# Optimization experiments

Measured on AMD Instinct MI355X. Metric: run time of the kernel, lower is better.

Reference implementation:

```python
import jax, jax.numpy as jnp
import numpy as np

WS = 32          # window_size; N = WS*WS tokens
NH = 8           # num_heads
HD = 64          # head_dim
DIM = 512        # model dim (= NH*HD)
B = 16
N = WS * WS


def _rel_index() -> np.ndarray:
    """Relative position index, identical to the torch __init__ construction."""
    coords = np.stack(np.meshgrid(np.arange(WS), np.arange(WS), indexing='ij'))
    coords = coords.reshape(2, -1)                       # [2, N]
    rel = coords[:, :, None] - coords[:, None, :]        # [2, N, N]
    rel = rel.transpose(1, 2, 0).copy()                  # [N, N, 2]
    rel[..., 0] += WS - 1
    rel[..., 1] += WS - 1
    rel[..., 0] *= 2 * WS - 1
    return rel.sum(-1).astype(np.int32)                  # [N, N], values in [0, (2WS-1)^2)


def setup_inputs() -> dict:
    key = jax.random.key(0)
    ks = jax.random.split(key, 5)
    s = DIM ** -0.5
    return {
        "x": jax.random.normal(ks[0], (B, N, DIM), jnp.float32),
        "qkv_w": jax.random.normal(ks[1], (3 * NH * HD, DIM), jnp.float32) * s,
        "qkv_b": jnp.zeros((3 * NH * HD,), jnp.float32),
        "proj_w": jax.random.normal(ks[2], (DIM, NH * HD), jnp.float32) * s,
        "proj_b": jnp.zeros((DIM,), jnp.float32),
        "bias_table": jax.random.normal(ks[3], ((2 * WS - 1) ** 2, NH), jnp.float32) * 0.02,
        "rel_index": jnp.asarray(_rel_index()),
    }


def reference(x, qkv_w, qkv_b, proj_w, proj_b, bias_table, rel_index):
    Bb, Nn, C = x.shape
    qkv = (x @ qkv_w.T + qkv_b).reshape(Bb, Nn, 3, NH, HD)
    q, k, v = jnp.moveaxis(qkv, 2, 0)                    # each [B, N, NH, HD]
    q = q * (HD ** -0.5)
    attn = jnp.einsum('bnhd,bmhd->bhnm', q, k)           # [B, NH, N, N]
    bias = bias_table[rel_index]                         # gather -> [N, N, NH]
    attn = attn + jnp.transpose(bias, (2, 0, 1))[None]
    attn = jax.nn.softmax(attn, axis=-1)                 # dropout p=0 (eval)
    out = jnp.einsum('bhnm,bmhd->bnhd', attn, v).reshape(Bb, Nn, NH * HD)
    out = out @ proj_w.T + proj_b                        # [B, N, DIM]
    return jnp.transpose(out, (0, 2, 1)).reshape(Bb, DIM, WS, WS)
```

## Files before the change

### kernel.cpp

```cpp
#include <hip/hip_runtime.h>
#include <hip/hip_bf16.h>


typedef __attribute__((ext_vector_type(4))) float  f32x4;
typedef __attribute__((ext_vector_type(8))) short  s16x8;
typedef __attribute__((ext_vector_type(4))) short  s16x4;

#define LOG2E 1.44269504f

__device__ __forceinline__ short f2bf(float f) {
    union { float f; unsigned u; } v; v.f = f;
    unsigned r = v.u + 0x7fffu + ((v.u >> 16) & 1u);
    return (short)(r >> 16);
}
__device__ __forceinline__ float u2f(unsigned u) {
    union { unsigned u; float f; } v; v.u = u; return v.f;
}
__device__ __forceinline__ unsigned cvtpk(float lo, float hi) {
    unsigned r;
    asm("v_cvt_pk_bf16_f32 %0, %1, %2" : "=v"(r) : "v"(lo), "v"(hi));
    return r;
}
__device__ __forceinline__ void gl_lds16(const short* g, short* l) {
    __builtin_amdgcn_global_load_lds(
        (const __attribute__((address_space(1))) unsigned int*)g,
        (__attribute__((address_space(3))) unsigned int*)l,
        16, 0, 0);
}
__device__ __forceinline__ void barrier_lgkm() {
    asm volatile("s_waitcnt lgkmcnt(0)" ::: "memory");
    __builtin_amdgcn_s_barrier();
}

__global__ void cvt_kernel(const float* __restrict__ src, short* __restrict__ dst) {
    int i = blockIdx.x * 256 + threadIdx.x;
    f32x4 v = ((const f32x4*)src)[i];
    s16x4 o;
    o[0]=f2bf(v[0]); o[1]=f2bf(v[1]); o[2]=f2bf(v[2]); o[3]=f2bf(v[3]);
    ((s16x4*)dst)[i] = o;
}

__global__ void bias_expand(const float* __restrict__ table, const int* __restrict__ ridx,
                            short* __restrict__ out) {
    int i = blockIdx.x * 256 + threadIdx.x;
    int n = i >> 10, m = i & 1023;
    int idx = ridx[i];
    const float* t = table + idx * 8;
    int pos = ((n*8 + (m >> 7))*4 + ((m >> 2) & 3))*32 + ((m >> 4) & 7)*4 + (m & 3);
    #pragma unroll
    for (int h = 0; h < 8; h++)
        out[h * 1048576 + pos] = f2bf(t[h] * LOG2E);
}

__global__ __launch_bounds__(256) void qkv_gemm(
    const short* __restrict__ Xb, const short* __restrict__ W,
    const float* __restrict__ bias,
    short* __restrict__ qb, short* __restrict__ kb, short* __restrict__ vtb)
{
    __shared__ __align__(16) short smem[8192];
    short* As = smem;
    short* Bs = smem + 4096;
    const int tid = threadIdx.x;
    const int lane = tid & 63, w = tid >> 6;
    const int quad = lane >> 4, l16 = lane & 15;
    const int m0 = blockIdx.y * 128, n0 = blockIdx.x * 128;
    const int wm = (w >> 1) * 64, wn = (w & 1) * 64;
    f32x4 acc[4][4] = {};

    const int ri = lane >> 2;
    const int u  = lane & 3;

    for (int k0 = 0; k0 < 512; k0 += 32) {
        __syncthreads();
        #pragma unroll
        for (int q = 0; q < 2; q++) {
            int rb = w*32 + q*16;
            int r  = rb + ri;
            int cu = u ^ ((r >> 1) & 3);
            gl_lds16(Xb + (m0 + r)*512 + k0 + cu*8, As + rb*32);
            gl_lds16(W  + (n0 + r)*512 + k0 + cu*8, Bs + rb*32);
        }
        __syncthreads();
        s16x8 af[4], bfr[4];
        #pragma unroll
        for (int i = 0; i < 4; i++) {
            int row = wm + i*16 + l16;
            af[i] = *(const s16x8*)(As + row*32 + (quad ^ ((row >> 1) & 3))*8);
        }
        #pragma unroll
        for (int j = 0; j < 4; j++) {
            int row = wn + j*16 + l16;
            bfr[j] = *(const s16x8*)(Bs + row*32 + (quad ^ ((row >> 1) & 3))*8);
        }
        #pragma unroll
        for (int i = 0; i < 4; i++)
            #pragma unroll
            for (int j = 0; j < 4; j++)
                acc[i][j] = __builtin_amdgcn_mfma_f32_16x16x32_bf16(af[i], bfr[j], acc[i][j], 0, 0, 0);
    }

    #pragma unroll
    for (int j = 0; j < 4; j++) {
        int col = n0 + wn + j*16 + l16;
        int which = col >> 9, rem = col & 511, h = rem >> 6, d = rem & 63;
        float bv = bias[col];
        #pragma unroll
        for (int i = 0; i < 4; i++) {
            int row = m0 + wm + i*16 + quad*4;
            int bi = row >> 10, n = row & 1023;
            if (which == 2) {
                float v0 = acc[i][j][0] + bv, v1 = acc[i][j][1] + bv;
                float v2 = acc[i][j][2] + bv, v3 = acc[i][j][3] + bv;
                uint2 pk; pk.x = cvtpk(v0, v1); pk.y = cvtpk(v2, v3);
                *(uint2*)&vtb[((bi*8 + h)*64 + d)*1024 + n] = pk;
            } else {
                #pragma unroll
                for (int r = 0; r < 4; r++) {
                    float v = acc[i][j][r] + bv;
                    if (which == 0)
                        qb[((bi*8 + h)*1024 + n + r)*64 + d] = f2bf(v * (0.125f * LOG2E));
                    else
                        kb[((bi*8 + h)*1024 + n + r)*64 + d] = f2bf(v);
                }
            }
        }
    }
}

__global__ __launch_bounds__(512, 4) void attn_kernel(
    const short* __restrict__ qbuf, const short* __restrict__ kbuf,
    const short* __restrict__ vtbuf, const short* __restrict__ bxp,
    short* __restrict__ ao)
{
    __shared__ __align__(16) short smem[26112];
    short* R1 = smem;
    short* Vs = smem + 17408;

    const int bh = blockIdx.y;
    const int b = bh >> 3, h = bh & 7;
    const int q0 = blockIdx.x * 128;
    const int tid = threadIdx.x, lane = tid & 63, w = tid >> 6;
    const int quad = lane >> 4, l16 = lane & 15;

    const short* qg = qbuf + (bh*1024 + q0) * 64;
    const short* kg = kbuf + bh * 65536;
    const short* vg = vtbuf + bh * 65536;

    const int kr = tid >> 3, ku = tid & 7;
    const int vr = tid >> 4, vu = tid & 15;

    {
        s16x8 qa = *(const s16x8*)(qg + kr*64 + ku*8);
        s16x8 qb2 = *(const s16x8*)(qg + (kr+64)*64 + ku*8);
        *(s16x8*)&R1[kr*72 + ku*8] = qa;
        *(s16x8*)&R1[(kr+64)*72 + ku*8] = qb2;
    }
    barrier_lgkm();
    s16x8 aq0 = *(const s16x8*)&R1[(w*16 + l16)*72 + quad*8];
    s16x8 aq1 = *(const s16x8*)&R1[(w*16 + l16)*72 + 32 + quad*8];

    s16x8 kv0 = *(const s16x8*)(kg + kr*64 + ku*8);
    s16x8 kv1 = *(const s16x8*)(kg + (kr+64)*64 + ku*8);
    s16x8 vv0 = *(const s16x8*)(vg + vr*1024 + vu*8);
    s16x8 vv1 = *(const s16x8*)(vg + (vr+32)*1024 + vu*8);

    float mrow = -1e30f, lrow = 0.f;
    f32x4 oacc[4] = {};
    short* Pw = R1 + w * 2176;
    const short* bbase = bxp + h*1048576 + ((q0 + w*16 + l16)*8)*128 + quad*32;

    for (int it = 0; it < 8; it++) {
        barrier_lgkm();

        uint4 bw[4];
        {
            const uint4* bp = (const uint4*)(bbase + it*128);
            bw[0]=bp[0]; bw[1]=bp[1]; bw[2]=bp[2]; bw[3]=bp[3];
        }

        *(s16x8*)&R1[kr*72 + ku*8]        = kv0;
        *(s16x8*)&R1[(kr+64)*72 + ku*8]   = kv1;
        *(s16x8*)&Vs[vr*136 + vu*8]       = vv0;
        *(s16x8*)&Vs[(vr+32)*136 + vu*8]  = vv1;

        if (it < 7) {
            const short* kg2 = kg + (it+1)*8192;
            kv0 = *(const s16x8*)(kg2 + kr*64 + ku*8);
            kv1 = *(const s16x8*)(kg2 + (kr+64)*64 + ku*8);
            vv0 = *(const s16x8*)(vg + vr*1024 + (it+1)*128 + vu*8);
            vv1 = *(const s16x8*)(vg + (vr+32)*1024 + (it+1)*128 + vu*8);
        }
        barrier_lgkm();

        f32x4 s[8];
        __builtin_amdgcn_s_setprio(1);
        #pragma unroll
        for (int nf = 0; nf < 8; nf++) {
            unsigned ua = (nf & 1) ? bw[nf >> 1].z : bw[nf >> 1].x;
            unsigned ub = (nf & 1) ? bw[nf >> 1].w : bw[nf >> 1].y;
            s[nf][0] = u2f(ua << 16); s[nf][1] = u2f(ua & 0xffff0000u);
            s[nf][2] = u2f(ub << 16); s[nf][3] = u2f(ub & 0xffff0000u);
            s16x8 bk0 = *(const s16x8*)&R1[(nf*16 + l16)*72 + quad*8];
            s16x8 bk1 = *(const s16x8*)&R1[(nf*16 + l16)*72 + 32 + quad*8];
            s[nf] = __builtin_amdgcn_mfma_f32_16x16x32_bf16(bk0, aq0, s[nf], 0, 0, 0);
            s[nf] = __builtin_amdgcn_mfma_f32_16x16x32_bf16(bk1, aq1, s[nf], 0, 0, 0);
        }
        __builtin_amdgcn_s_setprio(0);

        float mx = s[0][0];
        #pragma unroll
        for (int nf = 0; nf < 8; nf++) {
            float a = fmaxf(s[nf][0], s[nf][1]), c = fmaxf(s[nf][2], s[nf][3]);
            mx = fmaxf(mx, fmaxf(a, c));
        }
        if (!__all(mx - mrow <= 8.0f)) {
            float mr = fmaxf(mx, __shfl_xor(mx, 16));
            mr = fmaxf(mr, __shfl_xor(mr, 32));
            float mnew = fmaxf(mrow, mr);
            float alpha = __builtin_exp2f(mrow - mnew);
            mrow = mnew;
            lrow *= alpha;
            float a_r[4];
            #pragma unroll
            for (int r = 0; r < 4; r++) a_r[r] = __shfl(alpha, quad*4 + r);
            #pragma unroll
            for (int df = 0; df < 4; df++)
                #pragma unroll
                for (int r = 0; r < 4; r++)
                    oacc[df][r] *= a_r[r];
        }
        float rs = 0.f;
        #pragma unroll
        for (int nf = 0; nf < 8; nf++)
            #pragma unroll
            for (int r = 0; r < 4; r++) {
                float p = __builtin_exp2f(s[nf][r] - mrow);
                s[nf][r] = p;
                rs += p;
            }
        lrow += rs;

        barrier_lgkm();

        #pragma unroll
        for (int nf = 0; nf < 8; nf++) {
            uint2 pk;
            pk.x = cvtpk(s[nf][0], s[nf][1]);
            pk.y = cvtpk(s[nf][2], s[nf][3]);
            *(uint2*)&Pw[l16*136 + nf*16 + quad*4] = pk;
        }
        asm volatile("s_waitcnt lgkmcnt(0)" ::: "memory");

        __builtin_amdgcn_s_setprio(1);
        #pragma unroll
        for (int ks = 0; ks < 4; ks++) {
            s16x8 ap = *(const s16x8*)&Pw[l16*136 + ks*32 + quad*8];
            #pragma unroll
            for (int df = 0; df < 4; df++) {
                s16x8 bv = *(const s16x8*)&Vs[(df*16 + l16)*136 + ks*32 + quad*8];
                oacc[df] = __builtin_amdgcn_mfma_f32_16x16x32_bf16(ap, bv, oacc[df], 0, 0, 0);
            }
        }
        __builtin_amdgcn_s_setprio(0);
    }

    lrow += __shfl_xor(lrow, 16);
    lrow += __shfl_xor(lrow, 32);
    float inv_r[4];
    #pragma unroll
    for (int r = 0; r < 4; r++) inv_r[r] = 1.0f / __shfl(lrow, quad*4 + r);
    #pragma unroll
    for (int r = 0; r < 4; r++) {
        int n = q0 + w*16 + quad*4 + r;
        #pragma unroll
        for (int df = 0; df < 4; df++)
            ao[(b*1024 + n)*512 + h*64 + df*16 + l16] = f2bf(oacc[df][r] * inv_r[r]);
    }
}

__global__ __launch_bounds__(256) void proj_gemm(
    const short* __restrict__ A, const short* __restrict__ W,
    const float* __restrict__ bias, float* __restrict__ out)
{
    __shared__ __align__(16) short smemp[8448];
    short* As = smemp;
    short* Bs = smemp + 4096;
    const int tid = threadIdx.x;
    const int lane = tid & 63, w = tid >> 6;
    const int quad = lane >> 4, l16 = lane & 15;
    const int m0 = blockIdx.y * 128, n0 = blockIdx.x * 128;
    const int wm = (w >> 1) * 64, wn = (w & 1) * 64;
    f32x4 acc[4][4] = {};

    const int ri = lane >> 2;
    const int u  = lane & 3;

    for (int k0 = 0; k0 < 512; k0 += 32) {
        __syncthreads();
        #pragma unroll
        for (int q = 0; q < 2; q++) {
            int rb = w*32 + q*16;
            int r  = rb + ri;
            int cu = u ^ ((r >> 1) & 3);
            gl_lds16(A + (m0 + r)*512 + k0 + cu*8, As + rb*32);
            gl_lds16(W + (n0 + r)*512 + k0 + cu*8, Bs + rb*32);
        }
        __syncthreads();
        s16x8 af[4], bfr[4];
        #pragma unroll
        for (int i = 0; i < 4; i++) {
            int row = wm + i*16 + l16;
            af[i] = *(const s16x8*)(As + row*32 + (quad ^ ((row >> 1) & 3))*8);
        }
        #pragma unroll
        for (int j = 0; j < 4; j++) {
            int row = wn + j*16 + l16;
            bfr[j] = *(const s16x8*)(Bs + row*32 + (quad ^ ((row >> 1) & 3))*8);
        }
        #pragma unroll
        for (int i = 0; i < 4; i++)
            #pragma unroll
            for (int j = 0; j < 4; j++)
                acc[i][j] = __builtin_amdgcn_mfma_f32_16x16x32_bf16(af[i], bfr[j], acc[i][j], 0, 0, 0);
    }

    const int bi = m0 >> 10, nbase = m0 & 1023;
    float* Ts = (float*)smemp;
    #pragma unroll
    for (int ci = 0; ci < 4; ci++) {
        __syncthreads();
        if ((w & 1) == (ci >> 1)) {
            #pragma unroll
            for (int jj = 0; jj < 2; jj++) {
                int j = (ci & 1) * 2 + jj;
                int c = n0 + wn + j*16 + l16;
                float bv = bias[c];
                int cl = jj*16 + l16;
                #pragma unroll
                for (int i = 0; i < 4; i++) {
                    f32x4 v = acc[i][j];
                    v[0] += bv; v[1] += bv; v[2] += bv; v[3] += bv;
                    *(f32x4*)&Ts[cl*132 + wm + i*16 + quad*4] = v;
                }
            }
        }
        __syncthreads();
        #pragma unroll
        for (int p = 0; p < 4; p++) {
            int row = (tid >> 5) + p*8, col = (tid & 31)*4;
            f32x4 v = *(const f32x4*)&Ts[row*132 + col];
            *(f32x4*)&out[(bi*512 + n0 + ci*32 + row)*1024 + nbase + col] = v;
        }
    }
}

extern "C" void kernel_launch(void* const* d_in, const int* in_sizes, int n_in,
                              void* d_out, int out_size, void* d_ws, size_t ws_size,
                              hipStream_t stream) {
    const float* x      = (const float*)d_in[0];
    const float* qkv_w  = (const float*)d_in[1];
    const float* qkv_b  = (const float*)d_in[2];
    const float* proj_w = (const float*)d_in[3];
    const float* proj_b = (const float*)d_in[4];
    const float* btab   = (const float*)d_in[5];
    const int*   ridx   = (const int*)d_in[6];
    float* out = (float*)d_out;

    short* ws    = (short*)d_ws;
    short* wqkv  = ws;
    short* wproj = wqkv + 1536*512;
    short* qb    = wproj + 512*512;
    short* kb    = qb  + 16*8*1024*64;
    short* vtb   = kb  + 16*8*1024*64;
    short* bx    = vtb + 16*8*1024*64;
    short* ao    = bx  + 8*1024*1024;
    short* xb    = ao;

    cvt_kernel<<<8192, 256, 0, stream>>>(x, xb);
    cvt_kernel<<<768, 256, 0, stream>>>(qkv_w, wqkv);
    cvt_kernel<<<256, 256, 0, stream>>>(proj_w, wproj);
    bias_expand<<<4096, 256, 0, stream>>>(btab, ridx, bx);
    qkv_gemm<<<dim3(12, 128), 256, 0, stream>>>(xb, wqkv, qkv_b, qb, kb, vtb);
    attn_kernel<<<dim3(8, 128), 512, 0, stream>>>(qb, kb, vtb, bx, ao);
    proj_gemm<<<dim3(4, 128), 256, 0, stream>>>(ao, wproj, proj_b, out);
}
```

Measured before the change: 252.9 us.

## Halve attention key tile, raise occupancy, fuse prep kernels into one launch

The attention kernel now processes 64 keys per iteration instead of 128, which shrinks LDS use and register arrays so more blocks fit per CU (launch bounds raised to 8). The P buffer gets its own LDS region, so the barrier before writing P is dropped, and the bias layout is re-tiled to match the 64-key tiles. The four conversion and bias-expansion launches are merged into one prep kernel to save launch overhead, and the row max uses v_max3. The cost is twice as many loop iterations and barriers per block, plus possible register spilling under the tighter launch bound.

```diff
diff --git a/kernel.cpp b/kernel.cpp
--- a/kernel.cpp
+++ b/kernel.cpp
@@ -20,6 +20,11 @@
     unsigned r;
     asm("v_cvt_pk_bf16_f32 %0, %1, %2" : "=v"(r) : "v"(lo), "v"(hi));
     return r;
+}
+__device__ __forceinline__ float max3f(float a, float b, float c) {
+    float d;
+    asm("v_max3_f32 %0, %1, %2, %3" : "=v"(d) : "v"(a), "v"(b), "v"(c));
+    return d;
 }
 __device__ __forceinline__ void gl_lds16(const short* g, short* l) {
     __builtin_amdgcn_global_load_lds(
@@ -32,24 +37,33 @@
     __builtin_amdgcn_s_barrier();
 }
 
-__global__ void cvt_kernel(const float* __restrict__ src, short* __restrict__ dst) {
-    int i = blockIdx.x * 256 + threadIdx.x;
-    f32x4 v = ((const f32x4*)src)[i];
-    s16x4 o;
-    o[0]=f2bf(v[0]); o[1]=f2bf(v[1]); o[2]=f2bf(v[2]); o[3]=f2bf(v[3]);
-    ((s16x4*)dst)[i] = o;
-}
-
-__global__ void bias_expand(const float* __restrict__ table, const int* __restrict__ ridx,
-                            short* __restrict__ out) {
-    int i = blockIdx.x * 256 + threadIdx.x;
-    int n = i >> 10, m = i & 1023;
-    int idx = ridx[i];
-    const float* t = table + idx * 8;
-    int pos = ((n*8 + (m >> 7))*4 + ((m >> 2) & 3))*32 + ((m >> 4) & 7)*4 + (m & 3);
-    #pragma unroll
-    for (int h = 0; h < 8; h++)
-        out[h * 1048576 + pos] = f2bf(t[h] * LOG2E);
+__global__ __launch_bounds__(256) void prep_kernel(
+    const float* __restrict__ x, const float* __restrict__ qkv_w,
+    const float* __restrict__ proj_w,
+    const float* __restrict__ table, const int* __restrict__ ridx,
+    short* __restrict__ xb, short* __restrict__ wqkv, short* __restrict__ wproj,
+    short* __restrict__ bx)
+{
+    int bid = blockIdx.x, tid = threadIdx.x;
+    if (bid < 9216) {
+        const float* src; short* dst; int i;
+        if (bid < 8192)      { src = x;      dst = xb;    i = bid * 256 + tid; }
+        else if (bid < 8960) { src = qkv_w;  dst = wqkv;  i = (bid - 8192) * 256 + tid; }
+        else                 { src = proj_w; dst = wproj; i = (bid - 8960) * 256 + tid; }
+        f32x4 v = ((const f32x4*)src)[i];
+        s16x4 o;
+        o[0]=f2bf(v[0]); o[1]=f2bf(v[1]); o[2]=f2bf(v[2]); o[3]=f2bf(v[3]);
+        ((s16x4*)dst)[i] = o;
+    } else {
+        int i = (bid - 9216) * 256 + tid;
+        int n = i >> 10, m = i & 1023;
+        int idx = ridx[i];
+        const float* t = table + idx * 8;
+        int pos = n*1024 + (m >> 6)*64 + ((m >> 2) & 3)*16 + ((m >> 4) & 3)*4 + (m & 3);
+        #pragma unroll
+        for (int h = 0; h < 8; h++)
+            bx[h * 1048576 + pos] = f2bf(t[h] * LOG2E);
+    }
 }
 
 __global__ __launch_bounds__(256) void qkv_gemm(
@@ -127,14 +141,14 @@
     }
 }
 
-__global__ __launch_bounds__(512, 4) void attn_kernel(
+__global__ __launch_bounds__(512, 8) void attn_kernel(
     const short* __restrict__ qbuf, const short* __restrict__ kbuf,
     const short* __restrict__ vtbuf, const short* __restrict__ bxp,
     short* __restrict__ ao)
 {
-    __shared__ __align__(16) short smem[26112];
-    short* R1 = smem;
-    short* Vs = smem + 17408;
+    __shared__ __align__(16) short smem[18432];
+    short* Ks = smem;
+    short* Vs = smem + 4608;
 
     const int bh = blockIdx.y;
     const int b = bh >> 3, h = bh & 7;
@@ -146,73 +160,67 @@
     const short* kg = kbuf + bh * 65536;
     const short* vg = vtbuf + bh * 65536;
 
-    const int kr = tid >> 3, ku = tid & 7;
-    const int vr = tid >> 4, vu = tid & 15;
+    const int sr = tid >> 3;
+    const int sc = (tid & 7) * 8;
 
     {
-        s16x8 qa = *(const s16x8*)(qg + kr*64 + ku*8);
-        s16x8 qb2 = *(const s16x8*)(qg + (kr+64)*64 + ku*8);
-        *(s16x8*)&R1[kr*72 + ku*8] = qa;
-        *(s16x8*)&R1[(kr+64)*72 + ku*8] = qb2;
-    }
+        s16x8 qa  = *(const s16x8*)(qg + sr*64 + sc);
+        s16x8 qb2 = *(const s16x8*)(qg + (sr+64)*64 + sc);
+        *(s16x8*)&smem[sr*72 + sc]      = qa;
+        *(s16x8*)&smem[(sr+64)*72 + sc] = qb2;
+    }
+    s16x8 kv = *(const s16x8*)(kg + sr*64 + sc);
+    s16x8 vv = *(const s16x8*)(vg + sr*1024 + sc);
+
     barrier_lgkm();
-    s16x8 aq0 = *(const s16x8*)&R1[(w*16 + l16)*72 + quad*8];
-    s16x8 aq1 = *(const s16x8*)&R1[(w*16 + l16)*72 + 32 + quad*8];
-
-    s16x8 kv0 = *(const s16x8*)(kg + kr*64 + ku*8);
-    s16x8 kv1 = *(const s16x8*)(kg + (kr+64)*64 + ku*8);
-    s16x8 vv0 = *(const s16x8*)(vg + vr*1024 + vu*8);
-    s16x8 vv1 = *(const s16x8*)(vg + (vr+32)*1024 + vu*8);
+    s16x8 aq0 = *(const s16x8*)&smem[(w*16 + l16)*72 + quad*8];
+    s16x8 aq1 = *(const s16x8*)&smem[(w*16 + l16)*72 + 32 + quad*8];
 
     float mrow = -1e30f, lrow = 0.f;
     f32x4 oacc[4] = {};
-    short* Pw = R1 + w * 2176;
-    const short* bbase = bxp + h*1048576 + ((q0 + w*16 + l16)*8)*128 + quad*32;
-
-    for (int it = 0; it < 8; it++) {
+    short* Pw = smem + 9216 + w*1152;
+    const short* bbase = bxp + h*1048576 + (q0 + w*16 + l16)*1024 + quad*16;
+
+    for (int it = 0; it < 16; it++) {
         barrier_lgkm();
 
-        uint4 bw[4];
+        uint4 bw0, bw1;
         {
-            const uint4* bp = (const uint4*)(bbase + it*128);
-            bw[0]=bp[0]; bw[1]=bp[1]; bw[2]=bp[2]; bw[3]=bp[3];
-        }
-
-        *(s16x8*)&R1[kr*72 + ku*8]        = kv0;
-        *(s16x8*)&R1[(kr+64)*72 + ku*8]   = kv1;
-        *(s16x8*)&Vs[vr*136 + vu*8]       = vv0;
-        *(s16x8*)&Vs[(vr+32)*136 + vu*8]  = vv1;
-
-        if (it < 7) {
-            const short* kg2 = kg + (it+1)*8192;
-            kv0 = *(const s16x8*)(kg2 + kr*64 + ku*8);
-            kv1 = *(const s16x8*)(kg2 + (kr+64)*64 + ku*8);
-            vv0 = *(const s16x8*)(vg + vr*1024 + (it+1)*128 + vu*8);
-            vv1 = *(const s16x8*)(vg + (vr+32)*1024 + (it+1)*128 + vu*8);
+            const uint4* bp = (const uint4*)(bbase + it*64);
+            bw0 = bp[0]; bw1 = bp[1];
+        }
+
+        *(s16x8*)&Ks[sr*72 + sc] = kv;
+        *(s16x8*)&Vs[sr*72 + sc] = vv;
+        if (it < 15) {
+            kv = *(const s16x8*)(kg + (it+1)*4096 + sr*64 + sc);
+            vv = *(const s16x8*)(vg + sr*1024 + (it+1)*64 + sc);
         }
         barrier_lgkm();
 
-        f32x4 s[8];
+        f32x4 s[4];
+        const unsigned bu[8] = { bw0.x, bw0.y, bw0.z, bw0.w, bw1.x, bw1.y, bw1.z, bw1.w };
         __builtin_amdgcn_s_setprio(1);
         #pragma unroll
-        for (int nf = 0; nf < 8; nf++) {
-            unsigned ua = (nf & 1) ? bw[nf >> 1].z : bw[nf >> 1].x;
-            unsigned ub = (nf & 1) ? bw[nf >> 1].w : bw[nf >> 1].y;
+        for (int nf = 0; nf < 4; nf++) {
+            unsigned ua = bu[nf*2], ub = bu[nf*2 + 1];
             s[nf][0] = u2f(ua << 16); s[nf][1] = u2f(ua & 0xffff0000u);
             s[nf][2] = u2f(ub << 16); s[nf][3] = u2f(ub & 0xffff0000u);
-            s16x8 bk0 = *(const s16x8*)&R1[(nf*16 + l16)*72 + quad*8];
-            s16x8 bk1 = *(const s16x8*)&R1[(nf*16 + l16)*72 + 32 + quad*8];
+            s16x8 bk0 = *(const s16x8*)&Ks[(nf*16 + l16)*72 + quad*8];
+            s16x8 bk1 = *(const s16x8*)&Ks[(nf*16 + l16)*72 + 32 + quad*8];
             s[nf] = __builtin_amdgcn_mfma_f32_16x16x32_bf16(bk0, aq0, s[nf], 0, 0, 0);
             s[nf] = __builtin_amdgcn_mfma_f32_16x16x32_bf16(bk1, aq1, s[nf], 0, 0, 0);
         }
         __builtin_amdgcn_s_setprio(0);
 
-        float mx = s[0][0];
-        #pragma unroll
-        for (int nf = 0; nf < 8; nf++) {
-            float a = fmaxf(s[nf][0], s[nf][1]), c = fmaxf(s[nf][2], s[nf][3]);
-            mx = fmaxf(mx, fmaxf(a, c));
-        }
+        float mx = max3f(s[0][0], s[0][1], s[0][2]);
+        mx = max3f(mx, s[0][3], s[1][0]);
+        mx = max3f(mx, s[1][1], s[1][2]);
+        mx = max3f(mx, s[1][3], s[2][0]);
+        mx = max3f(mx, s[2][1], s[2][2]);
+        mx = max3f(mx, s[2][3], s[3][0]);
+        mx = max3f(mx, s[3][1], s[3][2]);
+        mx = fmaxf(mx, s[3][3]);
         if (!__all(mx - mrow <= 8.0f)) {
             float mr = fmaxf(mx, __shfl_xor(mx, 16));
             mr = fmaxf(mr, __shfl_xor(mr, 32));
@@ -231,7 +239,7 @@
         }
         float rs = 0.f;
         #pragma unroll
-        for (int nf = 0; nf < 8; nf++)
+        for (int nf = 0; nf < 4; nf++)
             #pragma unroll
             for (int r = 0; r < 4; r++) {
                 float p = __builtin_exp2f(s[nf][r] - mrow);
@@ -240,24 +248,22 @@
             }
         lrow += rs;
 
-        barrier_lgkm();
-
-        #pragma unroll
-        for (int nf = 0; nf < 8; nf++) {
+        #pragma unroll
+        for (int nf = 0; nf < 4; nf++) {
             uint2 pk;
             pk.x = cvtpk(s[nf][0], s[nf][1]);
             pk.y = cvtpk(s[nf][2], s[nf][3]);
-            *(uint2*)&Pw[l16*136 + nf*16 + quad*4] = pk;
+            *(uint2*)&Pw[l16*72 + nf*16 + quad*4] = pk;
         }
         asm volatile("s_waitcnt lgkmcnt(0)" ::: "memory");
 
         __builtin_amdgcn_s_setprio(1);
         #pragma unroll
-        for (int ks = 0; ks < 4; ks++) {
-            s16x8 ap = *(const s16x8*)&Pw[l16*136 + ks*32 + quad*8];
+        for (int ks = 0; ks < 2; ks++) {
+            s16x8 ap = *(const s16x8*)&Pw[l16*72 + ks*32 + quad*8];
             #pragma unroll
             for (int df = 0; df < 4; df++) {
-                s16x8 bv = *(const s16x8*)&Vs[(df*16 + l16)*136 + ks*32 + quad*8];
+                s16x8 bv = *(const s16x8*)&Vs[(df*16 + l16)*72 + ks*32 + quad*8];
                 oacc[df] = __builtin_amdgcn_mfma_f32_16x16x32_bf16(ap, bv, oacc[df], 0, 0, 0);
             }
         }
@@ -376,10 +382,7 @@
     short* ao    = bx  + 8*1024*1024;
     short* xb    = ao;
 
-    cvt_kernel<<<8192, 256, 0, stream>>>(x, xb);
-    cvt_kernel<<<768, 256, 0, stream>>>(qkv_w, wqkv);
-    cvt_kernel<<<256, 256, 0, stream>>>(proj_w, wproj);
-    bias_expand<<<4096, 256, 0, stream>>>(btab, ridx, bx);
+    prep_kernel<<<13312, 256, 0, stream>>>(x, qkv_w, proj_w, btab, ridx, xb, wqkv, wproj, bx);
     qkv_gemm<<<dim3(12, 128), 256, 0, stream>>>(xb, wqkv, qkv_b, qb, kb, vtb);
     attn_kernel<<<dim3(8, 128), 512, 0, stream>>>(qb, kb, vtb, bx, ao);
     proj_gemm<<<dim3(4, 128), 256, 0, stream>>>(ao, wproj, proj_b, out);
```

New measurement: 323.8 us. 1.28x slower.
